# Optimization experiments

Hardware: AMD Instinct MI355X
Metric: run time of the kernel (lower is better)

Reference implementation:

```python
import jax, jax.numpy as jnp
import numpy as np

B, N, E, F_IN, F_OUT, HEADS, HDIM = 64, 1024, 16384, 300, 8, 4, 32
ALPHA = 0.5
BETA = float(np.log(0.1 / 2 + 1.0))  # GCN2Conv: theta=0.1, layer=2


def _norm(src, dst, ew, n):
    # GCN normalization with added self loops: D^-1/2 (A + I) D^-1/2, edge-list form
    idx = jnp.arange(n)
    r = jnp.concatenate([src, idx])
    c = jnp.concatenate([dst, idx])
    w = jnp.concatenate([ew, jnp.ones((n,), ew.dtype)])
    deg = jax.ops.segment_sum(w, c, num_segments=n)  # deg >= 1 (self loop weight 1)
    dinv = jax.lax.rsqrt(jnp.maximum(deg, 1e-12))
    return r, c, dinv[r] * w * dinv[c]


def _prop(h, r, c, w, n):
    # out[c] += w * h[r]  (source-to-target message passing)
    return jax.ops.segment_sum(w[:, None] * h[r], c, num_segments=n)


def _forward(edge_index, x, edge_weight, W1, b1, W2, b2, W3, b3, W4, b4, Wl, Wr, att, bg, Wg1, Wm, bm, Wg2, Wp1, bp1, Wp2, bp2, Wo, bo):
    def per_graph(xg, ei, ewg):
        src, dst = ei[0], ei[1]
        n = xg.shape[0]
        r, c, w = _norm(src, dst, ewg, n)                    # weighted gcn norm
        r1, c1, w1 = _norm(src, dst, jnp.ones_like(ewg), n)  # unweighted gcn norm
        h1 = jax.nn.relu(_prop(xg @ W1, r, c, w, n) + b1)    # [n,256]
        h2 = jax.nn.relu(_prop(h1 @ W2, r, c, w, n) + b2)    # [n,128]
        h = jax.nn.relu(_prop(h2 @ W3, r, c, w, n) + b3)     # [n,64]
        h = jax.nn.relu(_prop(h @ W4, r, c, w, n) + b4)      # [n,32]
        # GATv2Conv(32, 32, heads=4), self loops, concat heads, eval mode (no dropout)
        idx = jnp.arange(n)
        s2, d2 = jnp.concatenate([src, idx]), jnp.concatenate([dst, idx])
        xl = (h @ Wl).reshape(n, HEADS, HDIM)  # source transform
        xr = (h @ Wr).reshape(n, HEADS, HDIM)  # target transform
        e = jax.nn.leaky_relu(xl[s2] + xr[d2], 0.2)          # [E2,H,C]
        lg = jnp.einsum('ehc,hc->eh', e, att)                # [E2,H]
        mx = jax.ops.segment_max(lg, d2, num_segments=n)
        a = jnp.exp(lg - mx[d2])
        alpha = a / jax.ops.segment_sum(a, d2, num_segments=n)[d2]
        h = jax.ops.segment_sum(alpha[..., None] * xl[s2], d2, num_segments=n).reshape(n, HEADS * HDIM) + bg
        h = jax.nn.relu(h)                                   # [n,128]
        # GCN2Conv(128, alpha=0.5, theta=0.1, layer=2), x0 = h2, shared weights, no bias
        z = (1.0 - ALPHA) * _prop(h, r, c, w, n) + ALPHA * h2
        h = jax.nn.relu((1.0 - BETA) * z + BETA * (z @ Wg1))
        # GCNConv(128, 256) called WITHOUT edge weights
        h = jax.nn.relu(_prop(h @ Wm, r1, c1, w1, n) + bm)
        # GCN2Conv(256, 0.5, 0.1, 2), x0 = h1
        z = (1.0 - ALPHA) * _prop(h, r, c, w, n) + ALPHA * h1
        h = jax.nn.relu((1.0 - BETA) * z + BETA * (z @ Wg2))  # [n,256]
        # dense_diff_pool stage 1: GCNConv(256,5) soft assignments + to_dense_adj
        s = jax.nn.softmax(_prop(h @ Wp1, r, c, w, n) + bp1, axis=-1)  # [n,5]
        adj = jnp.zeros((n, n), h.dtype).at[src, dst].add(ewg)
        nodes = s.T @ h                                      # [5,256]
        adj2 = s.T @ adj @ s                                 # [5,5]
        # DenseGCNConv(256,1): set diag to 1, sym-normalize, propagate
        di = jnp.arange(5)
        adjl = adj2.at[di, di].set(1.0)
        dd = jax.lax.rsqrt(jnp.maximum(adjl.sum(-1), 1.0))
        sc = jax.nn.softmax((dd[:, None] * adjl * dd[None, :]) @ (nodes @ Wp2) + bp2, axis=-1)  # [5,1]
        # dense_diff_pool stage 2
        return (sc.T @ nodes)[0]                             # [256]

    pooled = jax.vmap(per_graph)(x, edge_index, edge_weight)  # [B,256]
    return pooled @ Wo + bo


def setup_inputs():
    key = jax.random.key(0)
    ks = jax.random.split(key, 32)
    lin = lambda k, fi, fo: jax.random.normal(k, (fi, fo), jnp.float32) / np.sqrt(fi)
    return {
        'x': jax.random.normal(ks[0], (B, N, F_IN), jnp.float32),
        'edge_index': jax.random.randint(ks[1], (B, 2, E), 0, N),
        'edge_weight': jax.random.uniform(ks[2], (B, E), jnp.float32),
        'W1': lin(ks[3], F_IN, 256), 'b1': jnp.zeros((256,), jnp.float32),
        'W2': lin(ks[4], 256, 128), 'b2': jnp.zeros((128,), jnp.float32),
        'W3': lin(ks[5], 128, 64), 'b3': jnp.zeros((64,), jnp.float32),
        'W4': lin(ks[6], 64, 32), 'b4': jnp.zeros((32,), jnp.float32),
        'Wl': lin(ks[7], 32, 128), 'Wr': lin(ks[8], 32, 128),
        'att': jax.random.normal(ks[9], (HEADS, HDIM), jnp.float32) / np.sqrt(HDIM),
        'bg': jnp.zeros((128,), jnp.float32),
        'Wg1': lin(ks[10], 128, 128),
        'Wm': lin(ks[11], 128, 256), 'bm': jnp.zeros((256,), jnp.float32),
        'Wg2': lin(ks[12], 256, 256),
        'Wp1': lin(ks[13], 256, 5), 'bp1': jnp.zeros((5,), jnp.float32),
        'Wp2': lin(ks[14], 256, 1), 'bp2': jnp.zeros((1,), jnp.float32),
        'Wo': lin(ks[15], 256, F_OUT), 'bo': jnp.zeros((F_OUT,), jnp.float32),
    }


def reference(x, edge_index, edge_weight, W1, b1, W2, b2, W3, b3, W4, b4, Wl, Wr, att, bg, Wg1, Wm, bm, Wg2, Wp1, bp1, Wp2, bp2, Wo, bo):
    return _forward(edge_index, x, edge_weight, W1, b1, W2, b2, W3, b3, W4, b4, Wl, Wr, att, bg, Wg1, Wm, bm, Wg2, Wp1, bp1, Wp2, bp2, Wo, bo)
```

## Files before the change

### kernel.cpp

```cpp
#include <hip/hip_runtime.h>
#include <cstdint>
#include <cstddef>

constexpr int NB = 64;
constexpr int NN = 1024;
constexpr int NE = 16384;
constexpr int NCH = 16;
constexpr int CHE = NE / NCH;
constexpr float C_BETA = 0.04879016417f;

typedef __attribute__((ext_vector_type(8))) short s8v;
typedef __attribute__((ext_vector_type(4))) float f4v;

__device__ inline float bf2f(ushort u){ union{uint u;float f;} v; v.u=((uint)u)<<16; return v.f; }
__device__ inline ushort f2bf(float f){ union{float f;uint u;} v; v.f=f; uint r=v.u+0x7fffu+((v.u>>16)&1u); return (ushort)(r>>16); }
__device__ inline void up8(uint4 x, float* o){
  o[0]=bf2f((ushort)x.x); o[1]=bf2f((ushort)(x.x>>16));
  o[2]=bf2f((ushort)x.y); o[3]=bf2f((ushort)(x.y>>16));
  o[4]=bf2f((ushort)x.z); o[5]=bf2f((ushort)(x.z>>16));
  o[6]=bf2f((ushort)x.w); o[7]=bf2f((ushort)(x.w>>16));
}
__device__ inline uint pk2(float a, float b){ return (uint)f2bf(a) | ((uint)f2bf(b)<<16); }
__device__ inline uint4 pk8(const float* f){
  uint4 v; v.x=pk2(f[0],f[1]); v.y=pk2(f[2],f[3]); v.z=pk2(f[4],f[5]); v.w=pk2(f[6],f[7]); return v;
}
__device__ inline int swz8(int bid, int bpg){
  int xcd = bid & 7, j = bid >> 3;
  return (xcd * (NB/8) + j / bpg) * bpg + (j % bpg);
}


__global__ __launch_bounds__(256) void hist_k(const int* __restrict__ ei,
    const float* __restrict__ ew, int* __restrict__ phist, float* __restrict__ pdegw) {
  int blk = blockIdx.x;
  int b = blk & 63, ch = blk >> 6;
  __shared__ int hc[NN];
  __shared__ float hw[NN];
  int t = threadIdx.x;
  for (int i = t; i < NN; i += 256) { hc[i] = 0; hw[i] = 0.f; }
  __syncthreads();
  const int* dstb = ei + (size_t)b * 2 * NE + NE + ch * CHE;
  const float* ewb = ew + (size_t)b * NE + ch * CHE;
  for (int e = t; e < CHE; e += 256) {
    int d = dstb[e];
    atomicAdd(&hc[d], 1);
    atomicAdd(&hw[d], ewb[e]);
  }
  __syncthreads();
  size_t o = ((size_t)b * NCH + ch) * NN;
  for (int i = t; i < NN; i += 256) {
    phist[o + i] = hc[i];
    pdegw[o + i] = hw[i];
  }
}

__global__ __launch_bounds__(1024) void scan2_k(int* __restrict__ phist,
    const float* __restrict__ pdegw, float* __restrict__ dinvw,
    float* __restrict__ dinvu, int* __restrict__ rowptr) {
  int b = blockIdx.x, t = threadIdx.x;
  size_t base = (size_t)b * NCH * NN;
  int h[NCH];
  int cnt = 0; float dw = 1.0f;
#pragma unroll
  for (int c = 0; c < NCH; ++c) {
    h[c] = phist[base + c * NN + t];
    cnt += h[c];
    dw += pdegw[base + c * NN + t];
  }
  dinvw[b * NN + t] = rsqrtf(dw);
  dinvu[b * NN + t] = rsqrtf(1.0f + (float)cnt);
  __shared__ int ss[NN];
  ss[t] = cnt;
  __syncthreads();
  for (int off = 1; off < NN; off <<= 1) {
    int xv = (t >= off) ? ss[t - off] : 0;
    __syncthreads();
    ss[t] += xv;
    __syncthreads();
  }
  rowptr[b * (NN + 1) + t + 1] = ss[t];
  if (t == 0) rowptr[b * (NN + 1)] = 0;
  int excl = ss[t] - cnt;
#pragma unroll
  for (int c = 0; c < NCH; ++c) {
    phist[base + c * NN + t] = excl;
    excl += h[c];
  }
}

__global__ __launch_bounds__(256) void scatter2_k(const int* __restrict__ ei,
    const float* __restrict__ ew, const int* __restrict__ coff,
    const float* __restrict__ dinvw, int2* __restrict__ peW) {
  int blk = blockIdx.x;
  int b = blk & 63, ch = blk >> 6;
  __shared__ int sbase[NN];
  __shared__ int sfill[NN];
  __shared__ float sdw[NN];
  int t = threadIdx.x;
  for (int i = t; i < NN; i += 256) {
    sbase[i] = coff[((size_t)b * NCH + ch) * NN + i];
    sfill[i] = 0;
    sdw[i] = dinvw[b * NN + i];
  }
  __syncthreads();
  const int* srcb = ei + (size_t)b * 2 * NE + ch * CHE;
  const int* dstb = ei + (size_t)b * 2 * NE + NE + ch * CHE;
  const float* ewb = ew + (size_t)b * NE + ch * CHE;
  int2* pwb = peW + (size_t)b * NE;
  for (int e = t; e < CHE; e += 256) {
    int s = srcb[e], d = dstb[e];
    int pos = sbase[d] + atomicAdd(&sfill[d], 1);
    pwb[pos] = make_int2(s, __float_as_int(sdw[s] * ewb[e] * sdw[d]));
  }
}


__device__ inline void wcv(const float* __restrict__ W, ushort* __restrict__ Wt,
                           int idx, int K, int N, int Kp) {
  int n = idx / Kp, k = idx % Kp;
  Wt[idx] = (k < K) ? f2bf(W[(size_t)k * N + n]) : (ushort)0;
}

__global__ void wconv_all_k(const float* W1, const float* W2, const float* W3,
                            const float* W4, const float* Wl, const float* Wr,
                            const float* Wg1, const float* Wm, const float* Wg2,
                            ushort* Wt1, ushort* Wt2, ushort* Wt3, ushort* Wt4,
                            ushort* WtLR, ushort* Wtg1, ushort* Wtm, ushort* Wtg2) {
  int bb = blockIdx.x, t = threadIdx.x;
  if      (bb < 320) wcv(W1, Wt1, bb * 256 + t, 300, 256, 320);
  else if (bb < 448) wcv(W2, Wt2, (bb - 320) * 256 + t, 256, 128, 256);
  else if (bb < 480) wcv(W3, Wt3, (bb - 448) * 256 + t, 128, 64, 128);
  else if (bb < 488) wcv(W4, Wt4, (bb - 480) * 256 + t, 64, 32, 64);
  else if (bb < 504) wcv(Wl, WtLR, (bb - 488) * 256 + t, 32, 128, 32);
  else if (bb < 520) wcv(Wr, WtLR + 128 * 32, (bb - 504) * 256 + t, 32, 128, 32);
  else if (bb < 584) wcv(Wg1, Wtg1, (bb - 520) * 256 + t, 128, 128, 128);
  else if (bb < 712) wcv(Wm, Wtm, (bb - 584) * 256 + t, 128, 256, 128);
  else               wcv(Wg2, Wtg2, (bb - 712) * 256 + t, 256, 256, 256);
}


template<int WR, int NI, int MODE, int AF32>
__global__ __launch_bounds__(256) void mgemm_k(const ushort* __restrict__ A,
    const float* __restrict__ Af, const ushort* __restrict__ Bt,
    const ushort* __restrict__ Z, ushort* __restrict__ C, int M, int K, int N) {
  constexpr int BM = WR * 32;
  constexpr int BN = NI * 32;
  constexpr int KR = 300;
  __shared__ ushort As[BM][40];
  __shared__ ushort Bs[BN][40];
  int tid = threadIdx.x;
  int wave = tid >> 6, lane = tid & 63;
  int bm = blockIdx.y * BM, bn = blockIdx.x * BN;
  int wm = (wave >> 1) * (WR * 16), wn = (wave & 1) * (NI * 16);
  f4v acc[WR][NI];
#pragma unroll
  for (int a = 0; a < WR; ++a)
#pragma unroll
    for (int b = 0; b < NI; ++b)
#pragma unroll
      for (int q = 0; q < 4; ++q) acc[a][b][q] = 0.f;
  int r = lane & 15, kg = (lane >> 4) * 8;
  for (int k0 = 0; k0 < K; k0 += 32) {
#pragma unroll
    for (int c = tid; c < BM * 4; c += 256) {
      int row = c >> 2, kc = (c & 3) * 8;
      if (AF32) {
        const float* xr = Af + (size_t)(bm + row) * KR + k0 + kc;
        float f[8];
        if (k0 + kc + 8 <= KR) {
          float4 a = *(const float4*)xr;
          float4 bq = *(const float4*)(xr + 4);
          f[0]=a.x; f[1]=a.y; f[2]=a.z; f[3]=a.w;
          f[4]=bq.x; f[5]=bq.y; f[6]=bq.z; f[7]=bq.w;
        } else {
#pragma unroll
          for (int j = 0; j < 8; ++j) f[j] = (k0 + kc + j < KR) ? xr[j] : 0.f;
        }
        *(uint4*)&As[row][kc] = pk8(f);
      } else {
        *(uint4*)&As[row][kc] = *(const uint4*)&A[(size_t)(bm + row) * K + k0 + kc];
      }
    }
#pragma unroll
    for (int c = tid; c < BN * 4; c += 256) {
      int col = c >> 2, kc = (c & 3) * 8;
      *(uint4*)&Bs[col][kc] = *(const uint4*)&Bt[(size_t)(bn + col) * K + k0 + kc];
    }
    __syncthreads();
    s8v af[WR], bf[NI];
#pragma unroll
    for (int mi = 0; mi < WR; ++mi) af[mi] = *(const s8v*)&As[wm + mi * 16 + r][kg];
#pragma unroll
    for (int ni = 0; ni < NI; ++ni) bf[ni] = *(const s8v*)&Bs[wn + ni * 16 + r][kg];
#pragma unroll
    for (int mi = 0; mi < WR; ++mi)
#pragma unroll
      for (int ni = 0; ni < NI; ++ni)
        acc[mi][ni] = __builtin_amdgcn_mfma_f32_16x16x32_bf16(af[mi], bf[ni], acc[mi][ni], 0, 0, 0);
    __syncthreads();
  }
  int col = lane & 15, rowg = (lane >> 4) * 4;
#pragma unroll
  for (int mi = 0; mi < WR; ++mi)
#pragma unroll
    for (int ni = 0; ni < NI; ++ni)
#pragma unroll
      for (int q = 0; q < 4; ++q) {
        int row = bm + wm + mi * 16 + rowg + q;
        int cc = bn + wn + ni * 16 + col;
        size_t idx = (size_t)row * N + cc;
        float v = acc[mi][ni][q];
        if (MODE == 2) v = fmaxf((1.f - C_BETA) * bf2f(Z[idx]) + C_BETA * v, 0.f);
        C[idx] = f2bf(v);
      }
}


template<int D, int MODE, int WSEL>
__global__ __launch_bounds__(256) void prop_k(const ushort* __restrict__ in,
    ushort* __restrict__ out, const int2* __restrict__ pedge,
    const float* __restrict__ dinv, const int* __restrict__ rowptr,
    const float* __restrict__ bias, const ushort* __restrict__ x0) {
  constexpr int TPN = D / 8, NPB = 256 / TPN, BPG = NN / NPB;
  int t = threadIdx.x;
  int bid = swz8(blockIdx.x, BPG);
  int tn = t / TPN, cl = t % TPN;
  int node = bid * NPB + tn;
  int b = node >> 10, i = node & 1023;
  float di = dinv[node];
  float f[8], acc[8];
  uint4 ov = *(const uint4*)&in[(size_t)node * D + cl * 8];
  up8(ov, f);
  float w0 = di * di;
#pragma unroll
  for (int j = 0; j < 8; ++j) acc[j] = w0 * f[j];
  int r0 = rowptr[b * (NN + 1) + i], r1 = rowptr[b * (NN + 1) + i + 1];
  const int2* pe = pedge + (size_t)b * NE;
  const float* dvb = dinv + b * NN;
  const ushort* inb = in + (size_t)b * NN * D;
  int p = r0;
  for (; p + 4 <= r1; p += 4) {
    int2 e0 = pe[p], e1 = pe[p + 1], e2 = pe[p + 2], e3 = pe[p + 3];
    float wa, wb2, wc, wd;
    if (WSEL == 0) {
      wa = __int_as_float(e0.y); wb2 = __int_as_float(e1.y);
      wc = __int_as_float(e2.y); wd = __int_as_float(e3.y);
    } else {
      wa = dvb[e0.x] * di; wb2 = dvb[e1.x] * di;
      wc = dvb[e2.x] * di; wd = dvb[e3.x] * di;
    }
    uint4 rv0 = *(const uint4*)&inb[(size_t)e0.x * D + cl * 8];
    uint4 rv1 = *(const uint4*)&inb[(size_t)e1.x * D + cl * 8];
    uint4 rv2 = *(const uint4*)&inb[(size_t)e2.x * D + cl * 8];
    uint4 rv3 = *(const uint4*)&inb[(size_t)e3.x * D + cl * 8];
    up8(rv0, f);
#pragma unroll
    for (int j = 0; j < 8; ++j) acc[j] += wa * f[j];
    up8(rv1, f);
#pragma unroll
    for (int j = 0; j < 8; ++j) acc[j] += wb2 * f[j];
    up8(rv2, f);
#pragma unroll
    for (int j = 0; j < 8; ++j) acc[j] += wc * f[j];
    up8(rv3, f);
#pragma unroll
    for (int j = 0; j < 8; ++j) acc[j] += wd * f[j];
  }
  for (; p < r1; ++p) {
    int2 e = pe[p];
    float w = (WSEL == 0) ? __int_as_float(e.y) : dvb[e.x] * di;
    uint4 rv = *(const uint4*)&inb[(size_t)e.x * D + cl * 8];
    up8(rv, f);
#pragma unroll
    for (int j = 0; j < 8; ++j) acc[j] += w * f[j];
  }
  size_t ob = (size_t)node * D + cl * 8;
  if (MODE == 0) {
#pragma unroll
    for (int j = 0; j < 8; ++j) acc[j] = fmaxf(acc[j] + bias[cl * 8 + j], 0.f);
  } else {
    uint4 xv = *(const uint4*)&x0[ob];
    up8(xv, f);
#pragma unroll
    for (int j = 0; j < 8; ++j) acc[j] = 0.5f * acc[j] + 0.5f * f[j];
  }
  *(uint4*)&out[ob] = pk8(acc);
}


#define GAT_UPD(P, FL)                                            \
  if (P > m + 8.f) {                           \
    float sc = __expf(m - P);                                     \
    den *= sc;                                                    \
    _Pragma("unroll")                                             \
    for (int j = 0; j < 8; ++j) acc[j] *= sc;                     \
    m = P;                                                        \
    den += 1.f;                                                   \
    _Pragma("unroll")                                             \
    for (int j = 0; j < 8; ++j) acc[j] += FL[j];                  \
  } else {                                                        \
    float ex = __expf(P - m);                                     \
    den += ex;                                                    \
    _Pragma("unroll")                                             \
    for (int j = 0; j < 8; ++j) acc[j] += ex * FL[j];             \
  }

__global__ __launch_bounds__(256) void gat_fused_k(const ushort* __restrict__ xlr,
    const int2* __restrict__ pedge, const int* __restrict__ rowptr,
    const float* __restrict__ att, const float* __restrict__ bg,
    ushort* __restrict__ out) {
  int bid = swz8(blockIdx.x, NN / 16);
  int t = threadIdx.x;
  int tn = t >> 4, cl = t & 15;
  int node = bid * 16 + tn;
  int b = node >> 10, i = node & 1023;
  int ch = cl * 8;
  int r0 = rowptr[b * (NN + 1) + i], r1 = rowptr[b * (NN + 1) + i + 1];
  const ushort* xb = xlr + (size_t)b * NN * 256;
  const int2* pe = pedge + (size_t)b * NE;
  float fr[8], at[8];
  {
    uint4 rv = *(const uint4*)&xb[(size_t)i * 256 + 128 + ch];
    up8(rv, fr);
#pragma unroll
    for (int j = 0; j < 8; ++j) at[j] = att[ch + j];
  }
  float m, den, acc[8];
  {
    float fs[8];
    uint4 sv = *(const uint4*)&xb[(size_t)i * 256 + ch];
    up8(sv, fs);
    float part = 0.f;
#pragma unroll
    for (int j = 0; j < 8; ++j) {
      float v = fs[j] + fr[j];
      part += fmaxf(v, 0.2f * v) * at[j];
    }
    part += __shfl_xor(part, 1);
    part += __shfl_xor(part, 2);
    m = part; den = 1.f;
#pragma unroll
    for (int j = 0; j < 8; ++j) acc[j] = fs[j];
  }
  float fl0[8], fl1[8];
  int p = r0;
  for (; p + 2 <= r1; p += 2) {
    int s0 = pe[p].x, s1 = pe[p + 1].x;
    uint4 v0 = *(const uint4*)&xb[(size_t)s0 * 256 + ch];
    uint4 v1 = *(const uint4*)&xb[(size_t)s1 * 256 + ch];
    up8(v0, fl0); up8(v1, fl1);
    float p0 = 0.f, p1 = 0.f;
#pragma unroll
    for (int j = 0; j < 8; ++j) {
      float a0 = fl0[j] + fr[j];
      float a1 = fl1[j] + fr[j];
      p0 += fmaxf(a0, 0.2f * a0) * at[j];
      p1 += fmaxf(a1, 0.2f * a1) * at[j];
    }
    p0 += __shfl_xor(p0, 1); p0 += __shfl_xor(p0, 2);
    p1 += __shfl_xor(p1, 1); p1 += __shfl_xor(p1, 2);
    GAT_UPD(p0, fl0)
    GAT_UPD(p1, fl1)
  }
  if (p < r1) {
    int s = pe[p].x;
    uint4 v0 = *(const uint4*)&xb[(size_t)s * 256 + ch];
    up8(v0, fl0);
    float p0 = 0.f;
#pragma unroll
    for (int j = 0; j < 8; ++j) {
      float a0 = fl0[j] + fr[j];
      p0 += fmaxf(a0, 0.2f * a0) * at[j];
    }
    p0 += __shfl_xor(p0, 1); p0 += __shfl_xor(p0, 2);
    GAT_UPD(p0, fl0)
  }
  float inv = 1.f / den;
#pragma unroll
  for (int j = 0; j < 8; ++j) acc[j] = fmaxf(acc[j] * inv + bg[ch + j], 0.f);
  *(uint4*)&out[(size_t)node * 128 + ch] = pk8(acc);
}


__global__ __launch_bounds__(256) void pool_part_k(const ushort* __restrict__ h7,
                                                   float* __restrict__ part) {
  int bid = blockIdx.x;
  int bgr = bid >> 3, seg = bid & 7;
  int t = threadIdx.x;
  int rg = t >> 5, cl = t & 31;
  const ushort* hb = h7 + (size_t)bgr * NN * 256;
  float a[8] = {};
  float f[8];
  for (int r = seg * 128 + rg; r < seg * 128 + 128; r += 8) {
    uint4 v = *(const uint4*)&hb[(size_t)r * 256 + cl * 8];
    up8(v, f);
#pragma unroll
    for (int j = 0; j < 8; ++j) a[j] += f[j];
  }
  __shared__ float red[8][256];
#pragma unroll
  for (int j = 0; j < 8; ++j) red[rg][cl * 8 + j] = a[j];
  __syncthreads();
  float s = 0.f;
#pragma unroll
  for (int g = 0; g < 8; ++g) s += red[g][t];
  part[(size_t)bid * 256 + t] = s;
}

__global__ __launch_bounds__(256) void pool_out_k(const float* __restrict__ part,
    const float* __restrict__ Wo, const float* __restrict__ bo, float* __restrict__ out) {
  int bgr = blockIdx.x, t = threadIdx.x;
  float s = 0.f;
#pragma unroll
  for (int g = 0; g < 8; ++g) s += part[(size_t)(bgr * 8 + g) * 256 + t];
  __shared__ float pv[256];
  pv[t] = s;
  __syncthreads();
  if (t < 8) {
    float o = bo[t];
    for (int c = 0; c < 256; ++c) o += pv[c] * Wo[c * 8 + t];
    out[bgr * 8 + t] = o;
  }
}

__global__ void zero_out_k(float* out, int n) {
  int g = blockIdx.x * 256 + threadIdx.x;
  if (g < n) out[g] = 0.f;
}


extern "C" void kernel_launch(void* const* d_in, const int* in_sizes, int n_in,
                              void* d_out, int out_size, void* d_ws, size_t ws_size,
                              hipStream_t stream) {
  const float* x   = (const float*)d_in[0];
  const int*   ei  = (const int*)d_in[1];
  const float* ew  = (const float*)d_in[2];
  const float* W1  = (const float*)d_in[3];
  const float* b1  = (const float*)d_in[4];
  const float* W2  = (const float*)d_in[5];
  const float* b2  = (const float*)d_in[6];
  const float* W3  = (const float*)d_in[7];
  const float* b3  = (const float*)d_in[8];
  const float* W4  = (const float*)d_in[9];
  const float* b4  = (const float*)d_in[10];
  const float* Wl  = (const float*)d_in[11];
  const float* Wr  = (const float*)d_in[12];
  const float* att = (const float*)d_in[13];
  const float* bg  = (const float*)d_in[14];
  const float* Wg1 = (const float*)d_in[15];
  const float* Wm  = (const float*)d_in[16];
  const float* bm  = (const float*)d_in[17];
  const float* Wg2 = (const float*)d_in[18];
  const float* Wo  = (const float*)d_in[23];
  const float* bo  = (const float*)d_in[24];
  float* out = (float*)d_out;

  const int M = NB * NN;

  char* wp = (char*)d_ws;
  size_t used = 0;
  auto alloc = [&](size_t bytes) -> void* {
    void* p = (void*)wp;
    size_t a = (bytes + 255) & ~(size_t)255;
    wp += a; used += a;
    return p;
  };
  float* dinvw = (float*)alloc((size_t)NB * NN * 4);
  float* dinvu = (float*)alloc((size_t)NB * NN * 4);
  int*   rowptr= (int*)alloc((size_t)NB * (NN + 1) * 4);
  int*   phist = (int*)alloc((size_t)NB * NCH * NN * 4);
  float* pdegw = (float*)alloc((size_t)NB * NCH * NN * 4);
  int2*  peW   = (int2*)alloc((size_t)NB * NE * 8);
  float* part  = (float*)alloc((size_t)NB * 8 * 256 * 4);
  ushort* Wt1  = (ushort*)alloc((size_t)256 * 320 * 2);
  ushort* Wt2  = (ushort*)alloc((size_t)128 * 256 * 2);
  ushort* Wt3  = (ushort*)alloc((size_t)64 * 128 * 2);
  ushort* Wt4  = (ushort*)alloc((size_t)32 * 64 * 2);
  ushort* WtLR = (ushort*)alloc((size_t)256 * 32 * 2);
  ushort* Wtg1 = (ushort*)alloc((size_t)128 * 128 * 2);
  ushort* Wtm  = (ushort*)alloc((size_t)256 * 128 * 2);
  ushort* Wtg2 = (ushort*)alloc((size_t)256 * 256 * 2);
  ushort* B1 = (ushort*)alloc((size_t)M * 256 * 2);
  ushort* B2 = (ushort*)alloc((size_t)M * 256 * 2);
  ushort* B3 = (ushort*)alloc((size_t)M * 256 * 2);
  ushort* B4 = (ushort*)alloc((size_t)M * 256 * 2);
  ushort* B2a = B2, *B2b = B2 + (size_t)M * 128;
  ushort* B3a = B3, *B3b = B3 + (size_t)M * 128;

  if (used > ws_size) {
    zero_out_k<<<(out_size + 255) / 256, 256, 0, stream>>>(out, out_size);
    return;
  }

  wconv_all_k<<<968, 256, 0, stream>>>(W1, W2, W3, W4, Wl, Wr, Wg1, Wm, Wg2,
                                       Wt1, Wt2, Wt3, Wt4, WtLR, Wtg1, Wtm, Wtg2);

  hist_k<<<NB * NCH, 256, 0, stream>>>(ei, ew, phist, pdegw);
  scan2_k<<<NB, 1024, 0, stream>>>(phist, pdegw, dinvw, dinvu, rowptr);
  scatter2_k<<<NB * NCH, 256, 0, stream>>>(ei, ew, phist, dinvw, peW);

  mgemm_k<2,4,0,1><<<dim3(2, M / 64), 256, 0, stream>>>(nullptr, x, Wt1, nullptr, B2, M, 320, 256);
  prop_k<256,0,0><<<M / 8, 256, 0, stream>>>(B2, B1, peW, dinvw, rowptr, b1, nullptr);
  mgemm_k<2,4,0,0><<<dim3(1, M / 64), 256, 0, stream>>>(B1, nullptr, Wt2, nullptr, B2a, M, 256, 128);
  prop_k<128,0,0><<<M / 16, 256, 0, stream>>>(B2a, B3a, peW, dinvw, rowptr, b2, nullptr);
  mgemm_k<2,2,0,0><<<dim3(1, M / 64), 256, 0, stream>>>(B3a, nullptr, Wt3, nullptr, B2a, M, 128, 64);
  prop_k<64,0,0><<<M / 32, 256, 0, stream>>>(B2a, B3b, peW, dinvw, rowptr, b3, nullptr);
  mgemm_k<2,1,0,0><<<dim3(1, M / 64), 256, 0, stream>>>(B3b, nullptr, Wt4, nullptr, B2a, M, 64, 32);
  prop_k<32,0,0><<<M / 64, 256, 0, stream>>>(B2a, B2b, peW, dinvw, rowptr, b4, nullptr);

  mgemm_k<2,4,0,0><<<dim3(2, M / 64), 256, 0, stream>>>(B2b, nullptr, WtLR, nullptr, B4, M, 32, 256);
  gat_fused_k<<<M / 16, 256, 0, stream>>>(B4, peW, rowptr, att, bg, B2a);

  prop_k<128,1,0><<<M / 16, 256, 0, stream>>>(B2a, B2b, peW, dinvw, rowptr, nullptr, B3a);
  mgemm_k<2,4,2,0><<<dim3(1, M / 64), 256, 0, stream>>>(B2b, nullptr, Wtg1, B2b, B2a, M, 128, 128);

  mgemm_k<2,4,0,0><<<dim3(2, M / 64), 256, 0, stream>>>(B2a, nullptr, Wtm, nullptr, B3, M, 128, 256);
  prop_k<256,0,1><<<M / 8, 256, 0, stream>>>(B3, B2, peW, dinvu, rowptr, bm, nullptr);

  prop_k<256,1,0><<<M / 8, 256, 0, stream>>>(B2, B3, peW, dinvw, rowptr, nullptr, B1);
  mgemm_k<2,4,2,0><<<dim3(2, M / 64), 256, 0, stream>>>(B3, nullptr, Wtg2, B3, B2, M, 256, 256);

  pool_part_k<<<NB * 8, 256, 0, stream>>>(B2, part);
  pool_out_k<<<NB, 256, 0, stream>>>(part, Wo, bo, out);
}
```

Before: 415.5 us.

## Prefetch next two K-tiles into registers to overlap global loads with MFMA

Restructures the bf16 MFMA GEMM main loop into a register double-buffered pipeline. Global loads for the K-tiles one and two steps ahead are issued into registers before the MFMA work on the current shared tile, then committed to LDS after a barrier. This is meant to hide global memory latency behind the matrix math, at the cost of extra registers and the assumption that BM*4 equals 256 threads' worth of A loads.

```diff
diff --git a/kernel.cpp b/kernel.cpp
--- a/kernel.cpp
+++ b/kernel.cpp
@@ -139,6 +139,43 @@
 }
 
 
+#define LOADSET(FA, PAW, PB0, PB1, KOFF)                                        \
+  if (AF32) {                                                                   \
+    const float* xr = Af + (size_t)(bm + arow) * KR + (KOFF) + akc;             \
+    if ((KOFF) + akc + 8 <= KR) {                                               \
+      float4 q1 = *(const float4*)xr, q2 = *(const float4*)(xr + 4);            \
+      FA[0]=q1.x; FA[1]=q1.y; FA[2]=q1.z; FA[3]=q1.w;                           \
+      FA[4]=q2.x; FA[5]=q2.y; FA[6]=q2.z; FA[7]=q2.w;                           \
+    } else {                                                                    \
+      _Pragma("unroll")                                                         \
+      for (int j = 0; j < 8; ++j) FA[j] = ((KOFF)+akc+j < KR) ? xr[j] : 0.f;    \
+    }                                                                           \
+  } else {                                                                      \
+    PAW = *(const uint4*)&A[(size_t)(bm + arow) * K + (KOFF) + akc];            \
+  }                                                                             \
+  if (tid < BCH) PB0 = *(const uint4*)&Bt[(size_t)(bn + arow) * K + (KOFF) + akc]; \
+  if (BCH > 256) PB1 = *(const uint4*)&Bt[(size_t)(bn + b1row) * K + (KOFF) + b1kc];
+
+#define COMMITSET(FA, PAW, PB0, PB1)               \
+  if (AF32) *(uint4*)&As[arow][akc] = pk8(FA);     \
+  else      *(uint4*)&As[arow][akc] = PAW;         \
+  if (tid < BCH) *(uint4*)&Bs[arow][akc] = PB0;    \
+  if (BCH > 256) *(uint4*)&Bs[b1row][b1kc] = PB1;
+
+#define DO_MFMA()                                                                \
+  {                                                                              \
+    s8v af[WR], bf[NI];                                                          \
+    _Pragma("unroll")                                                            \
+    for (int mi = 0; mi < WR; ++mi) af[mi] = *(const s8v*)&As[wm + mi*16 + r][kg]; \
+    _Pragma("unroll")                                                            \
+    for (int ni = 0; ni < NI; ++ni) bf[ni] = *(const s8v*)&Bs[wn + ni*16 + r][kg]; \
+    _Pragma("unroll")                                                            \
+    for (int mi = 0; mi < WR; ++mi)                                              \
+      _Pragma("unroll")                                                          \
+      for (int ni = 0; ni < NI; ++ni)                                            \
+        acc[mi][ni] = __builtin_amdgcn_mfma_f32_16x16x32_bf16(af[mi], bf[ni], acc[mi][ni], 0, 0, 0); \
+  }
+
 template<int WR, int NI, int MODE, int AF32>
 __global__ __launch_bounds__(256) void mgemm_k(const ushort* __restrict__ A,
     const float* __restrict__ Af, const ushort* __restrict__ Bt,
@@ -146,6 +183,7 @@
   constexpr int BM = WR * 32;
   constexpr int BN = NI * 32;
   constexpr int KR = 300;
+  constexpr int BCH = BN * 4;
   __shared__ ushort As[BM][40];
   __shared__ ushort Bs[BN][40];
   int tid = threadIdx.x;
@@ -159,46 +197,39 @@
     for (int b = 0; b < NI; ++b)
 #pragma unroll
       for (int q = 0; q < 4; ++q) acc[a][b][q] = 0.f;
+
+  int arow = tid >> 2, akc = (tid & 3) * 8;
+  int b1row = (256 + tid) >> 2, b1kc = ((256 + tid) & 3) * 8;
+
+  float fa0[8], fa1[8];
+  uint4 paw0, paw1;
+  uint4 pb00, pb10, pb01, pb11;
+
   int r = lane & 15, kg = (lane >> 4) * 8;
-  for (int k0 = 0; k0 < K; k0 += 32) {
-#pragma unroll
-    for (int c = tid; c < BM * 4; c += 256) {
-      int row = c >> 2, kc = (c & 3) * 8;
-      if (AF32) {
-        const float* xr = Af + (size_t)(bm + row) * KR + k0 + kc;
-        float f[8];
-        if (k0 + kc + 8 <= KR) {
-          float4 a = *(const float4*)xr;
-          float4 bq = *(const float4*)(xr + 4);
-          f[0]=a.x; f[1]=a.y; f[2]=a.z; f[3]=a.w;
-          f[4]=bq.x; f[5]=bq.y; f[6]=bq.z; f[7]=bq.w;
-        } else {
-#pragma unroll
-          for (int j = 0; j < 8; ++j) f[j] = (k0 + kc + j < KR) ? xr[j] : 0.f;
-        }
-        *(uint4*)&As[row][kc] = pk8(f);
-      } else {
-        *(uint4*)&As[row][kc] = *(const uint4*)&A[(size_t)(bm + row) * K + k0 + kc];
-      }
-    }
-#pragma unroll
-    for (int c = tid; c < BN * 4; c += 256) {
-      int col = c >> 2, kc = (c & 3) * 8;
-      *(uint4*)&Bs[col][kc] = *(const uint4*)&Bt[(size_t)(bn + col) * K + k0 + kc];
-    }
-    __syncthreads();
-    s8v af[WR], bf[NI];
-#pragma unroll
-    for (int mi = 0; mi < WR; ++mi) af[mi] = *(const s8v*)&As[wm + mi * 16 + r][kg];
-#pragma unroll
-    for (int ni = 0; ni < NI; ++ni) bf[ni] = *(const s8v*)&Bs[wn + ni * 16 + r][kg];
-#pragma unroll
-    for (int mi = 0; mi < WR; ++mi)
-#pragma unroll
-      for (int ni = 0; ni < NI; ++ni)
-        acc[mi][ni] = __builtin_amdgcn_mfma_f32_16x16x32_bf16(af[mi], bf[ni], acc[mi][ni], 0, 0, 0);
-    __syncthreads();
-  }
+
+  LOADSET(fa0, paw0, pb00, pb10, 0)
+  if (32 < K) { LOADSET(fa1, paw1, pb01, pb11, 32) }
+
+  int k0 = 0;
+  for (; k0 + 64 <= K; k0 += 64) {
+    COMMITSET(fa0, paw0, pb00, pb10)
+    __syncthreads();
+    if (k0 + 64 < K) { LOADSET(fa0, paw0, pb00, pb10, k0 + 64) }
+    DO_MFMA()
+    __syncthreads();
+    COMMITSET(fa1, paw1, pb01, pb11)
+    __syncthreads();
+    if (k0 + 96 < K) { LOADSET(fa1, paw1, pb01, pb11, k0 + 96) }
+    DO_MFMA()
+    __syncthreads();
+  }
+  if (k0 < K) {
+    COMMITSET(fa0, paw0, pb00, pb10)
+    __syncthreads();
+    DO_MFMA()
+    __syncthreads();
+  }
+
   int col = lane & 15, rowg = (lane >> 4) * 4;
 #pragma unroll
   for (int mi = 0; mi < WR; ++mi)
```

Result: faster. 401.2 us (-3.4%).
